# Optimization experiments

Hardware: AMD Instinct MI355X
Metric: run time of the kernel (lower is better)

Reference implementation:

```python
import jax, jax.numpy as jnp
import numpy as np
import math

BBOX_XFORM_CLIP = math.log(1000.0 / 16.0)  # standard BoxCoder clip on dw/dh
WX, WY, WW, WH = 10.0, 10.0, 5.0, 5.0      # BoxCoder weights
TO_REMOVE = 1.0                             # legacy +1 box convention


def _decode(rel_codes, boxes):
    # boxes: [N,4] xyxy reference proposals; rel_codes: [N,4] deltas
    widths = boxes[:, 2] - boxes[:, 0] + TO_REMOVE
    heights = boxes[:, 3] - boxes[:, 1] + TO_REMOVE
    ctr_x = boxes[:, 0] + 0.5 * widths
    ctr_y = boxes[:, 1] + 0.5 * heights

    dx = rel_codes[:, 0] / WX
    dy = rel_codes[:, 1] / WY
    dw = jnp.minimum(rel_codes[:, 2] / WW, BBOX_XFORM_CLIP)
    dh = jnp.minimum(rel_codes[:, 3] / WH, BBOX_XFORM_CLIP)

    pred_ctr_x = dx * widths + ctr_x
    pred_ctr_y = dy * heights + ctr_y
    pred_w = jnp.exp(dw) * widths
    pred_h = jnp.exp(dh) * heights

    x1 = pred_ctr_x - 0.5 * pred_w
    y1 = pred_ctr_y - 0.5 * pred_h
    x2 = pred_ctr_x + 0.5 * pred_w - 1.0
    y2 = pred_ctr_y + 0.5 * pred_h - 1.0
    return jnp.stack([x1, y1, x2, y2], axis=1)


def setup_inputs() -> dict:
    key = jax.random.key(0)
    k1, k2, k3, k4 = jax.random.split(key, 4)
    N, C = 262144, 81
    W = H = 1024
    class_logits = jax.random.normal(k1, (N, C), dtype=jnp.float32)
    box_regression = jax.random.normal(k2, (N, 4), dtype=jnp.float32) * 0.5
    # valid xyxy proposals inside the image: x2 > x1, y2 > y1
    xy1 = jax.random.uniform(k3, (N, 2), dtype=jnp.float32) * (W - 64.0)
    wh = jax.random.uniform(k4, (N, 2), dtype=jnp.float32) * 60.0 + 2.0
    proposal_boxes = jnp.concatenate([xy1, xy1 + wh], axis=1)
    return {
        "class_logits": class_logits,
        "box_regression": box_regression,
        "proposal_boxes": proposal_boxes,
        "img_w": W,
        "img_h": H,
    }


def reference(class_logits, box_regression, proposal_boxes, img_w, img_h):
    # softmax over classes
    class_prob = jax.nn.softmax(class_logits, axis=-1)  # [N, C]
    rel = box_regression[:, -4:]
    proposals = _decode(rel, proposal_boxes)            # [N, 4]
    proposals = jnp.maximum(proposals, 0.0)             # proposals[proposals < 0] = 0
    C = class_prob.shape[1]
    # is_repeat path: repeat decoded box for every class, then per-row boxlist
    boxes = jnp.tile(proposals, (1, C)).reshape(-1, 4)  # [N*C, 4]
    # clip_to_image (remove_empty=False): clamp to [0, W-1] x [0, H-1]
    wmax = jnp.asarray(img_w - 1, dtype=boxes.dtype)
    hmax = jnp.asarray(img_h - 1, dtype=boxes.dtype)
    x1 = jnp.clip(boxes[:, 0], 0.0, wmax)
    y1 = jnp.clip(boxes[:, 1], 0.0, hmax)
    x2 = jnp.clip(boxes[:, 2], 0.0, wmax)
    y2 = jnp.clip(boxes[:, 3], 0.0, hmax)
    boxes = jnp.stack([x1, y1, x2, y2], axis=1)         # [N*C, 4]
    scores = class_prob.reshape(-1)                     # [N*C]
    return boxes, scores
```

## Files before the change

kernel.cpp:

```cpp
#include <hip/hip_runtime.h>
#include <math.h>

#define NUM_CLASSES 81

typedef float vfloat4 __attribute__((ext_vector_type(4)));

__device__ __forceinline__ float4 decode_clip(const float4 b, const float4 r,
                                              const float wmax, const float hmax)
{
    const float BBOX_XFORM_CLIP = 4.135166556742356f;
    const float w  = b.z - b.x + 1.0f;
    const float h  = b.w - b.y + 1.0f;
    const float cx = b.x + 0.5f * w;
    const float cy = b.y + 0.5f * h;
    const float dx = r.x * 0.1f;
    const float dy = r.y * 0.1f;
    const float dw = fminf(r.z * 0.2f, BBOX_XFORM_CLIP);
    const float dh = fminf(r.w * 0.2f, BBOX_XFORM_CLIP);
    const float px = dx * w + cx;
    const float py = dy * h + cy;
    const float pw = expf(dw) * w;
    const float ph = expf(dh) * h;
    const float x1 = fminf(fmaxf(px - 0.5f * pw, 0.0f), wmax);
    const float y1 = fminf(fmaxf(py - 0.5f * ph, 0.0f), hmax);
    const float x2 = fminf(fmaxf(px + 0.5f * pw - 1.0f, 0.0f), wmax);
    const float y2 = fminf(fmaxf(py + 0.5f * ph - 1.0f, 0.0f), hmax);
    return make_float4(x1, y1, x2, y2);
}

#define BROWS  64
#define BELEMS (BROWS * NUM_CLASSES)
#define BITERS (BELEMS / 256)

__global__ __launch_bounds__(256) void boxes_kernel(
    const float4* __restrict__ box_reg4,
    const float4* __restrict__ prop4,
    const int* __restrict__ img_w_p,
    const int* __restrict__ img_h_p,
    float* __restrict__ out_boxes,
    int N)
{
    __shared__ float4 lds_box[BROWS];
    const int tid  = threadIdx.x;
    const int row0 = blockIdx.x * BROWS;
    if (row0 >= N) return;
    const int rows = min(BROWS, N - row0);

    if (tid < rows) {
        const int row = row0 + tid;
        const float wmax = (float)(*img_w_p) - 1.0f;
        const float hmax = (float)(*img_h_p) - 1.0f;
        lds_box[tid] = decode_clip(prop4[row], box_reg4[row], wmax, hmax);
    }
    __syncthreads();

    vfloat4* dst = (vfloat4*)out_boxes + (size_t)row0 * NUM_CLASSES;
    if (rows == BROWS) {
        #pragma unroll
        for (int i = 0; i < BITERS; ++i) {
            const int j = tid + i * 256;
            const int rloc = (int)(((unsigned)j * 12946u) >> 20);
            const float4 bx = lds_box[rloc];
            vfloat4 bv = { bx.x, bx.y, bx.z, bx.w };
            __builtin_nontemporal_store(bv, dst + j);
        }
        if (tid < (BELEMS - BITERS * 256)) {
            const int j = BITERS * 256 + tid;
            const int rloc = (int)(((unsigned)j * 12946u) >> 20);
            const float4 bx = lds_box[rloc];
            vfloat4 bv = { bx.x, bx.y, bx.z, bx.w };
            __builtin_nontemporal_store(bv, dst + j);
        }
    } else {
        const int elems = rows * NUM_CLASSES;
        for (int i = 0; i <= BITERS; ++i) {
            const int j = tid + i * 256;
            if (j < elems) {
                const int rloc = (int)(((unsigned)j * 12946u) >> 20);
                const float4 bx = lds_box[rloc];
                vfloat4 bv = { bx.x, bx.y, bx.z, bx.w };
                __builtin_nontemporal_store(bv, dst + j);
            }
        }
    }
}

#define SROWS  16
#define SELEMS (SROWS * NUM_CLASSES)
#define SVECS  (SELEMS / 4)

__global__ __launch_bounds__(256) void scores_kernel(
    const float* __restrict__ logits,
    float* __restrict__ out_scores,
    int N)
{
    __shared__ vfloat4 lds4[SVECS];
    float* lds_val = (float*)lds4;
    const int tid  = threadIdx.x;
    const int row0 = blockIdx.x * SROWS;
    if (row0 >= N) return;
    const int rows = min(SROWS, N - row0);
    const bool full = (rows == SROWS);
    const int elems = rows * NUM_CLASSES;

    const float* lbase = logits + (size_t)row0 * NUM_CLASSES;
    if (full) {
        const vfloat4* lbase4 = (const vfloat4*)lbase;
        { int idx = tid;        lds4[idx] = lbase4[idx]; }
        { int idx = tid + 256;  if (idx < SVECS) lds4[idx] = lbase4[idx]; }
    } else {
        for (int i = 0; i < 6; ++i) {
            int e = tid + i * 256;
            if (e < elems) lds_val[e] = lbase[e];
        }
    }
    __syncthreads();

    const int sub = tid & 15;
    const int rl  = tid >> 4;
    if (rl < rows) {
        float* rowv = lds_val + rl * NUM_CLASSES;

        float v[6];
        float m = -INFINITY;
        #pragma unroll
        for (int i = 0; i < 6; ++i) {
            const int k = sub + i * 16;
            if (k < NUM_CLASSES) { v[i] = rowv[k]; m = fmaxf(m, v[i]); }
            else                 { v[i] = -INFINITY; }
        }
        #pragma unroll
        for (int off = 1; off <= 8; off <<= 1)
            m = fmaxf(m, __shfl_xor(m, off));

        float s = 0.0f;
        #pragma unroll
        for (int i = 0; i < 6; ++i) {
            const int k = sub + i * 16;
            if (k < NUM_CLASSES) { v[i] = __expf(v[i] - m); s += v[i]; }
        }
        #pragma unroll
        for (int off = 1; off <= 8; off <<= 1)
            s += __shfl_xor(s, off);

        const float inv = 1.0f / s;
        #pragma unroll
        for (int i = 0; i < 6; ++i) {
            const int k = sub + i * 16;
            if (k < NUM_CLASSES) rowv[k] = v[i] * inv;
        }
    }
    __syncthreads();

    float* sdst = out_scores + (size_t)row0 * NUM_CLASSES;
    if (full) {
        vfloat4* sdst4 = (vfloat4*)sdst;
        { int idx = tid;       __builtin_nontemporal_store(lds4[idx], sdst4 + idx); }
        { int idx = tid + 256; if (idx < SVECS)
                               __builtin_nontemporal_store(lds4[idx], sdst4 + idx); }
    } else {
        for (int i = 0; i < 6; ++i) {
            int e = tid + i * 256;
            if (e < elems) sdst[e] = lds_val[e];
        }
    }
}

extern "C" void kernel_launch(void* const* d_in, const int* in_sizes, int n_in,
                              void* d_out, int out_size, void* d_ws, size_t ws_size,
                              hipStream_t stream) {
    const float* logits   = (const float*)d_in[0];
    const float4* boxreg4 = (const float4*)d_in[1];
    const float4* prop4   = (const float4*)d_in[2];
    const int*   img_w_p  = (const int*)d_in[3];
    const int*   img_h_p  = (const int*)d_in[4];

    const int N = in_sizes[1] / 4;

    float* out_boxes  = (float*)d_out;
    float* out_scores = out_boxes + (size_t)N * NUM_CLASSES * 4;

    const int bblocks = (N + BROWS - 1) / BROWS;
    boxes_kernel<<<bblocks, 256, 0, stream>>>(
        boxreg4, prop4, img_w_p, img_h_p, out_boxes, N);

    const int sblocks = (N + SROWS - 1) / SROWS;
    scores_kernel<<<sblocks, 256, 0, stream>>>(logits, out_scores, N);
}
```

Before: 483.6 us.

## Fuse box broadcast and softmax kernels into one 64-row block kernel

```diff
diff --git a/kernel.cpp b/kernel.cpp
--- a/kernel.cpp
+++ b/kernel.cpp
@@ -2,6 +2,13 @@
 #include <math.h>
 
 #define NUM_CLASSES 81
+#define ROWS 64
+#define ELEMS (ROWS * NUM_CLASSES)
+#define VECS  (ELEMS / 4)
+#define LVEC_ITERS (VECS / 256)
+#define LVEC_REM   (VECS - LVEC_ITERS * 256)
+#define BOX_ITERS  (ELEMS / 256)
+#define BOX_REM    (ELEMS - BOX_ITERS * 256)
 
 typedef float vfloat4 __attribute__((ext_vector_type(4)));
 
@@ -28,140 +35,157 @@
     return make_float4(x1, y1, x2, y2);
 }
 
-#define BROWS  64
-#define BELEMS (BROWS * NUM_CLASSES)
-#define BITERS (BELEMS / 256)
-
-__global__ __launch_bounds__(256) void boxes_kernel(
+__device__ __forceinline__ void lds_barrier()
+{
+    asm volatile("s_waitcnt lgkmcnt(0)" ::: "memory");
+    __builtin_amdgcn_s_barrier();
+    __builtin_amdgcn_sched_barrier(0);
+}
+
+__global__ __launch_bounds__(256) void fused_kernel(
+    const float* __restrict__ logits,
     const float4* __restrict__ box_reg4,
     const float4* __restrict__ prop4,
     const int* __restrict__ img_w_p,
     const int* __restrict__ img_h_p,
     float* __restrict__ out_boxes,
+    float* __restrict__ out_scores,
     int N)
 {
-    __shared__ float4 lds_box[BROWS];
+    __shared__ float lds_val[ELEMS];
+    __shared__ float4 lds_box[ROWS];
+    vfloat4* lds4 = (vfloat4*)lds_val;
+
     const int tid  = threadIdx.x;
-    const int row0 = blockIdx.x * BROWS;
+    const int row0 = blockIdx.x * ROWS;
     if (row0 >= N) return;
-    const int rows = min(BROWS, N - row0);
-
-    if (tid < rows) {
-        const int row = row0 + tid;
-        const float wmax = (float)(*img_w_p) - 1.0f;
-        const float hmax = (float)(*img_h_p) - 1.0f;
-        lds_box[tid] = decode_clip(prop4[row], box_reg4[row], wmax, hmax);
-    }
-    __syncthreads();
-
-    vfloat4* dst = (vfloat4*)out_boxes + (size_t)row0 * NUM_CLASSES;
-    if (rows == BROWS) {
-        #pragma unroll
-        for (int i = 0; i < BITERS; ++i) {
+    const int rows = min(ROWS, N - row0);
+
+    const float wmax = (float)(*img_w_p) - 1.0f;
+    const float hmax = (float)(*img_h_p) - 1.0f;
+
+    if (rows == ROWS) {
+        const vfloat4* lbase4 = (const vfloat4*)(logits + (size_t)row0 * NUM_CLASSES);
+        vfloat4 lv[LVEC_ITERS];
+        #pragma unroll
+        for (int i = 0; i < LVEC_ITERS; ++i) lv[i] = lbase4[tid + i * 256];
+        vfloat4 lvr = {0.f, 0.f, 0.f, 0.f};
+        if (tid < LVEC_REM) lvr = lbase4[LVEC_ITERS * 256 + tid];
+
+        if (tid < ROWS) {
+            lds_box[tid] = decode_clip(prop4[row0 + tid], box_reg4[row0 + tid], wmax, hmax);
+        }
+        lds_barrier();
+
+        vfloat4* bdst = (vfloat4*)out_boxes + (size_t)row0 * NUM_CLASSES;
+        #pragma unroll
+        for (int i = 0; i < BOX_ITERS; ++i) {
             const int j = tid + i * 256;
             const int rloc = (int)(((unsigned)j * 12946u) >> 20);
             const float4 bx = lds_box[rloc];
             vfloat4 bv = { bx.x, bx.y, bx.z, bx.w };
-            __builtin_nontemporal_store(bv, dst + j);
-        }
-        if (tid < (BELEMS - BITERS * 256)) {
-            const int j = BITERS * 256 + tid;
+            __builtin_nontemporal_store(bv, bdst + j);
+        }
+        if (tid < BOX_REM) {
+            const int j = BOX_ITERS * 256 + tid;
             const int rloc = (int)(((unsigned)j * 12946u) >> 20);
             const float4 bx = lds_box[rloc];
             vfloat4 bv = { bx.x, bx.y, bx.z, bx.w };
-            __builtin_nontemporal_store(bv, dst + j);
-        }
+            __builtin_nontemporal_store(bv, bdst + j);
+        }
+
+        #pragma unroll
+        for (int i = 0; i < LVEC_ITERS; ++i) lds4[tid + i * 256] = lv[i];
+        if (tid < LVEC_REM) lds4[LVEC_ITERS * 256 + tid] = lvr;
+        lds_barrier();
+
+        {
+            const int sub = tid & 3;
+            const int rl  = tid >> 2;
+            float* rowv = lds_val + rl * NUM_CLASSES;
+
+            float v[21];
+            float m = -INFINITY;
+            #pragma unroll
+            for (int i = 0; i < 21; ++i) {
+                const int k = sub + i * 4;
+                if (k < NUM_CLASSES) { v[i] = rowv[k]; m = fmaxf(m, v[i]); }
+                else                 { v[i] = -INFINITY; }
+            }
+            m = fmaxf(m, __shfl_xor(m, 1));
+            m = fmaxf(m, __shfl_xor(m, 2));
+
+            float s = 0.0f;
+            #pragma unroll
+            for (int i = 0; i < 21; ++i) {
+                const int k = sub + i * 4;
+                if (k < NUM_CLASSES) { v[i] = __expf(v[i] - m); s += v[i]; }
+            }
+            s += __shfl_xor(s, 1);
+            s += __shfl_xor(s, 2);
+
+            const float inv = 1.0f / s;
+            #pragma unroll
+            for (int i = 0; i < 21; ++i) {
+                const int k = sub + i * 4;
+                if (k < NUM_CLASSES) rowv[k] = v[i] * inv;
+            }
+        }
+        lds_barrier();
+
+        vfloat4* sdst = (vfloat4*)(out_scores + (size_t)row0 * NUM_CLASSES);
+        #pragma unroll
+        for (int i = 0; i < LVEC_ITERS; ++i)
+            __builtin_nontemporal_store(lds4[tid + i * 256], sdst + tid + i * 256);
+        if (tid < LVEC_REM)
+            __builtin_nontemporal_store(lds4[LVEC_ITERS * 256 + tid],
+                                        sdst + LVEC_ITERS * 256 + tid);
     } else {
         const int elems = rows * NUM_CLASSES;
-        for (int i = 0; i <= BITERS; ++i) {
-            const int j = tid + i * 256;
-            if (j < elems) {
-                const int rloc = (int)(((unsigned)j * 12946u) >> 20);
-                const float4 bx = lds_box[rloc];
-                vfloat4 bv = { bx.x, bx.y, bx.z, bx.w };
-                __builtin_nontemporal_store(bv, dst + j);
-            }
-        }
-    }
-}
-
-#define SROWS  16
-#define SELEMS (SROWS * NUM_CLASSES)
-#define SVECS  (SELEMS / 4)
-
-__global__ __launch_bounds__(256) void scores_kernel(
-    const float* __restrict__ logits,
-    float* __restrict__ out_scores,
-    int N)
-{
-    __shared__ vfloat4 lds4[SVECS];
-    float* lds_val = (float*)lds4;
-    const int tid  = threadIdx.x;
-    const int row0 = blockIdx.x * SROWS;
-    if (row0 >= N) return;
-    const int rows = min(SROWS, N - row0);
-    const bool full = (rows == SROWS);
-    const int elems = rows * NUM_CLASSES;
-
-    const float* lbase = logits + (size_t)row0 * NUM_CLASSES;
-    if (full) {
-        const vfloat4* lbase4 = (const vfloat4*)lbase;
-        { int idx = tid;        lds4[idx] = lbase4[idx]; }
-        { int idx = tid + 256;  if (idx < SVECS) lds4[idx] = lbase4[idx]; }
-    } else {
-        for (int i = 0; i < 6; ++i) {
-            int e = tid + i * 256;
-            if (e < elems) lds_val[e] = lbase[e];
-        }
-    }
-    __syncthreads();
-
-    const int sub = tid & 15;
-    const int rl  = tid >> 4;
-    if (rl < rows) {
-        float* rowv = lds_val + rl * NUM_CLASSES;
-
-        float v[6];
-        float m = -INFINITY;
-        #pragma unroll
-        for (int i = 0; i < 6; ++i) {
-            const int k = sub + i * 16;
-            if (k < NUM_CLASSES) { v[i] = rowv[k]; m = fmaxf(m, v[i]); }
-            else                 { v[i] = -INFINITY; }
-        }
-        #pragma unroll
-        for (int off = 1; off <= 8; off <<= 1)
-            m = fmaxf(m, __shfl_xor(m, off));
-
-        float s = 0.0f;
-        #pragma unroll
-        for (int i = 0; i < 6; ++i) {
-            const int k = sub + i * 16;
-            if (k < NUM_CLASSES) { v[i] = __expf(v[i] - m); s += v[i]; }
-        }
-        #pragma unroll
-        for (int off = 1; off <= 8; off <<= 1)
-            s += __shfl_xor(s, off);
-
-        const float inv = 1.0f / s;
-        #pragma unroll
-        for (int i = 0; i < 6; ++i) {
-            const int k = sub + i * 16;
-            if (k < NUM_CLASSES) rowv[k] = v[i] * inv;
-        }
-    }
-    __syncthreads();
-
-    float* sdst = out_scores + (size_t)row0 * NUM_CLASSES;
-    if (full) {
-        vfloat4* sdst4 = (vfloat4*)sdst;
-        { int idx = tid;       __builtin_nontemporal_store(lds4[idx], sdst4 + idx); }
-        { int idx = tid + 256; if (idx < SVECS)
-                               __builtin_nontemporal_store(lds4[idx], sdst4 + idx); }
-    } else {
-        for (int i = 0; i < 6; ++i) {
-            int e = tid + i * 256;
-            if (e < elems) sdst[e] = lds_val[e];
+        const float* lbase = logits + (size_t)row0 * NUM_CLASSES;
+        for (int e = tid; e < elems; e += 256) lds_val[e] = lbase[e];
+        if (tid < rows) {
+            lds_box[tid] = decode_clip(prop4[row0 + tid], box_reg4[row0 + tid], wmax, hmax);
+        }
+        __syncthreads();
+
+        const int sub = tid & 3;
+        const int rl  = tid >> 2;
+        if (rl < rows) {
+            float* rowv = lds_val + rl * NUM_CLASSES;
+            float v[21];
+            float m = -INFINITY;
+            #pragma unroll
+            for (int i = 0; i < 21; ++i) {
+                const int k = sub + i * 4;
+                if (k < NUM_CLASSES) { v[i] = rowv[k]; m = fmaxf(m, v[i]); }
+                else                 { v[i] = -INFINITY; }
+            }
+            m = fmaxf(m, __shfl_xor(m, 1));
+            m = fmaxf(m, __shfl_xor(m, 2));
+            float s = 0.0f;
+            #pragma unroll
+            for (int i = 0; i < 21; ++i) {
+                const int k = sub + i * 4;
+                if (k < NUM_CLASSES) { v[i] = __expf(v[i] - m); s += v[i]; }
+            }
+            s += __shfl_xor(s, 1);
+            s += __shfl_xor(s, 2);
+            const float inv = 1.0f / s;
+            #pragma unroll
+            for (int i = 0; i < 21; ++i) {
+                const int k = sub + i * 4;
+                if (k < NUM_CLASSES) rowv[k] = v[i] * inv;
+            }
+        }
+        __syncthreads();
+
+        float* sdst = out_scores + (size_t)row0 * NUM_CLASSES;
+        for (int e = tid; e < elems; e += 256) sdst[e] = lds_val[e];
+        float4* bdst = (float4*)out_boxes + (size_t)row0 * NUM_CLASSES;
+        for (int j = tid; j < elems; j += 256) {
+            const int rloc = (int)(((unsigned)j * 12946u) >> 20);
+            bdst[j] = lds_box[rloc];
         }
     }
 }
@@ -180,10 +204,7 @@
     float* out_boxes  = (float*)d_out;
     float* out_scores = out_boxes + (size_t)N * NUM_CLASSES * 4;
 
-    const int bblocks = (N + BROWS - 1) / BROWS;
-    boxes_kernel<<<bblocks, 256, 0, stream>>>(
-        boxreg4, prop4, img_w_p, img_h_p, out_boxes, N);
-
-    const int sblocks = (N + SROWS - 1) / SROWS;
-    scores_kernel<<<sblocks, 256, 0, stream>>>(logits, out_scores, N);
-}
+    const int blocks = (N + ROWS - 1) / ROWS;
+    fused_kernel<<<blocks, 256, 0, stream>>>(
+        logits, boxreg4, prop4, img_w_p, img_h_p, out_boxes, out_scores, N);
+}
```

Measured after the change: 495.2 us. 2.4% more time.
